# Kernel optimization log

Hardware: AMD Instinct MI355X
Metric: run time of the kernel (lower is better)

The kernel has to match this reference:

```python
import jax, jax.numpy as jnp
import numpy as np


def setup_inputs() -> dict:
    key = jax.random.key(0)
    k1, k2 = jax.random.split(key)
    from_points = jax.random.normal(k1, (16384, 64), dtype=jnp.float32)
    to_points = jax.random.normal(k2, (16384, 64), dtype=jnp.float32)
    return {"from_points": from_points, "to_points": to_points}


def reference(from_points, to_points):
    # Squared L2 distance matrix [N, M] via ||a||^2 + ||b||^2 - 2 a.b,
    # avoiding the O(N*M*D) broadcasted intermediate of the original.
    a_sq = jnp.sum(from_points * from_points, axis=-1)          # [N]
    b_sq = jnp.sum(to_points * to_points, axis=-1)              # [M]
    cross = jnp.einsum('nd,md->nm', from_points, to_points)     # [N, M]
    dist_mat = a_sq[:, None] + b_sq[None, :] - 2.0 * cross      # [N, M]
    # Row-wise min (nearest neighbor squared distance), then sum.
    return jnp.sum(jnp.min(dist_mat, axis=1))
```

## Files before the change

### kernel.cpp

```cpp
#include <hip/hip_runtime.h>
#include <stdint.h>

#define N_PTS 16384
#define TSPLITS 32
#define NBLOCKS (256 * TSPLITS / 4)
#define TO_TILES 16

typedef __attribute__((ext_vector_type(8)))  short bf16x8;
typedef __attribute__((ext_vector_type(16))) float f32x16;

__device__ __forceinline__ unsigned short f2bf(float f) {
    unsigned u = __float_as_uint(f);
    u += 0x7FFFu + ((u >> 16) & 1u);
    return (unsigned short)(u >> 16);
}
__device__ __forceinline__ float tree16(f32x16 a) {
    float m0 = fminf(fminf(a[0],  a[1]),  a[2]);
    float m1 = fminf(fminf(a[3],  a[4]),  a[5]);
    float m2 = fminf(fminf(a[6],  a[7]),  a[8]);
    float m3 = fminf(fminf(a[9],  a[10]), a[11]);
    float m4 = fminf(fminf(a[12], a[13]), a[14]);
    float m5 = fminf(fminf(a[15], m0), m1);
    return fminf(fminf(fminf(m2, m3), m4), m5);
}

__global__ __launch_bounds__(256) void prep_kernel(
        const float* __restrict__ from_pts, const float* __restrict__ to_pts,
        float* __restrict__ a_sq, float* __restrict__ bsqp,
        unsigned short* __restrict__ BfF, unsigned short* __restrict__ AtoF,
        float* __restrict__ out) {
    int gid = blockIdx.x * 256 + threadIdx.x;
    int row = gid >> 3;
    int sub = gid & 7;
    bool isFrom = row < N_PTS;
    int r = row & (N_PTS - 1);
    const float* src = isFrom ? from_pts : to_pts;
    float4 v0 = ((const float4*)src)[r * 16 + sub * 2];
    float4 v1 = ((const float4*)src)[r * 16 + sub * 2 + 1];
    float s = v0.x*v0.x + v0.y*v0.y + v0.z*v0.z + v0.w*v0.w
            + v1.x*v1.x + v1.y*v1.y + v1.z*v1.z + v1.w*v1.w;
    s += __shfl_xor(s, 1); s += __shfl_xor(s, 2); s += __shfl_xor(s, 4);
    float sc = isFrom ? -2.0f : 1.0f;
    union { unsigned short u[8]; uint4 q; } w;
    w.u[0] = f2bf(v0.x * sc); w.u[1] = f2bf(v0.y * sc);
    w.u[2] = f2bf(v0.z * sc); w.u[3] = f2bf(v0.w * sc);
    w.u[4] = f2bf(v1.x * sc); w.u[5] = f2bf(v1.y * sc);
    w.u[6] = f2bf(v1.z * sc); w.u[7] = f2bf(v1.w * sc);
    int st = r >> 5;
    int m  = r & 31;
    int kb = sub >> 1, h = sub & 1;
    size_t fidx = (((size_t)st * 4 + kb) * 64 + h * 32 + m) * 8;
    if (isFrom) {
        *(uint4*)(BfF + fidx) = w.q;
        if (sub == 0) a_sq[r] = s;
    } else {
        *(uint4*)(AtoF + fidx) = w.q;
        if (sub == 0)
            bsqp[st * 32 + ((m >> 2) & 1) * 16 + (m & 3) + 4 * (m >> 3)] = s;
    }
    if (gid == 0) out[0] = 0.0f;
}

__global__ __launch_bounds__(256, 4) void main_kernel(
        const unsigned short* __restrict__ BfF,
        const unsigned short* __restrict__ AtoF,
        const float* __restrict__ bsqp, float* __restrict__ pmin) {
    __shared__ __align__(16) unsigned short abuf[2][2048];
    __shared__ __align__(16) float bsq_s[512];

    const int tid = threadIdx.x;
    const int lane = tid & 63;
    const int l31 = lane & 31;
    const int h   = lane >> 5;
    const int wv  = tid >> 6;
    const int wid = (blockIdx.x << 2) + wv;
    const int fg  = wid & 255;
    const int ts  = wid >> 8;

    const bf16x8* Bv = (const bf16x8*)BfF;

    bsq_s[tid]       = bsqp[ts * 512 + tid];
    bsq_s[tid + 256] = bsqp[ts * 512 + 256 + tid];

    bf16x8 Bf0[4], Bf1[4];
    #pragma unroll
    for (int kb = 0; kb < 4; kb++) {
        Bf0[kb] = Bv[((size_t)(2 * fg)     * 4 + kb) * 64 + lane];
        Bf1[kb] = Bv[((size_t)(2 * fg + 1) * 4 + kb) * 64 + lane];
    }

    const int gtb = ts * TO_TILES;
    auto stage = [&](int gt, int buf) {
        const unsigned short* g = AtoF + (((size_t)gt * 4 + wv) * 64 + lane) * 8;
        unsigned short* l = &abuf[buf][wv * 512];
        __builtin_amdgcn_global_load_lds(
            (const __attribute__((address_space(1))) unsigned int*)g,
            (__attribute__((address_space(3))) unsigned int*)l, 16, 0, 0);
    };

    float rmin0 = 3.0e38f, rmin1 = 3.0e38f;
    auto compute = [&](int tl, int cb) {
        bf16x8 A[4];
        #pragma unroll
        for (int kb = 0; kb < 4; kb++)
            A[kb] = *(const bf16x8*)&abuf[cb][kb * 512 + lane * 8];
        union { float4 f[4]; f32x16 v; } cu;
        const float4* cp = (const float4*)&bsq_s[tl * 32 + h * 16];
        cu.f[0] = cp[0]; cu.f[1] = cp[1]; cu.f[2] = cp[2]; cu.f[3] = cp[3];
        f32x16 acc0 = __builtin_amdgcn_mfma_f32_32x32x16_bf16(A[0], Bf0[0], cu.v, 0, 0, 0);
        acc0 = __builtin_amdgcn_mfma_f32_32x32x16_bf16(A[1], Bf0[1], acc0, 0, 0, 0);
        acc0 = __builtin_amdgcn_mfma_f32_32x32x16_bf16(A[2], Bf0[2], acc0, 0, 0, 0);
        acc0 = __builtin_amdgcn_mfma_f32_32x32x16_bf16(A[3], Bf0[3], acc0, 0, 0, 0);
        rmin0 = fminf(rmin0, tree16(acc0));
        f32x16 acc1 = __builtin_amdgcn_mfma_f32_32x32x16_bf16(A[0], Bf1[0], cu.v, 0, 0, 0);
        acc1 = __builtin_amdgcn_mfma_f32_32x32x16_bf16(A[1], Bf1[1], acc1, 0, 0, 0);
        acc1 = __builtin_amdgcn_mfma_f32_32x32x16_bf16(A[2], Bf1[2], acc1, 0, 0, 0);
        acc1 = __builtin_amdgcn_mfma_f32_32x32x16_bf16(A[3], Bf1[3], acc1, 0, 0, 0);
        rmin1 = fminf(rmin1, tree16(acc1));
    };

    stage(gtb, 0);
    __syncthreads();
    #pragma unroll 1
    for (int t = 0; t < TO_TILES - 1; t++) {
        stage(gtb + t + 1, (t + 1) & 1);
        compute(t, t & 1);
        __syncthreads();
    }
    compute(TO_TILES - 1, (TO_TILES - 1) & 1);

    rmin0 = fminf(rmin0, __shfl_xor(rmin0, 32));
    rmin1 = fminf(rmin1, __shfl_xor(rmin1, 32));
    if (lane < 32) {
        pmin[(size_t)ts * N_PTS + fg * 64 + l31]      = rmin0;
        pmin[(size_t)ts * N_PTS + fg * 64 + 32 + l31] = rmin1;
    }
}

__global__ __launch_bounds__(256) void finish_kernel(
        const float* __restrict__ a_sq, const float* __restrict__ pmin,
        float* __restrict__ out) {
    int r = blockIdx.x * 256 + threadIdx.x;
    float m = pmin[r];
    #pragma unroll
    for (int s = 1; s < TSPLITS; s++)
        m = fminf(m, pmin[(size_t)s * N_PTS + r]);
    float v = a_sq[r] + m;
    #pragma unroll
    for (int k = 1; k < 64; k <<= 1) v += __shfl_xor(v, k);
    __shared__ float red[4];
    if ((threadIdx.x & 63) == 0) red[threadIdx.x >> 6] = v;
    __syncthreads();
    if (threadIdx.x == 0)
        atomicAdd(out, red[0] + red[1] + red[2] + red[3]);
}

extern "C" void kernel_launch(void* const* d_in, const int* in_sizes, int n_in,
                              void* d_out, int out_size, void* d_ws, size_t ws_size,
                              hipStream_t stream) {
    const float* from_pts = (const float*)d_in[0];
    const float* to_pts   = (const float*)d_in[1];
    char* ws = (char*)d_ws;
    float*          a_sq = (float*)ws;
    float*          bsqp = (float*)(ws + (64 << 10));
    float*          pmin = (float*)(ws + (128 << 10));
    unsigned short* BfF  = (unsigned short*)(ws + (128 << 10) + (2 << 20));
    unsigned short* AtoF = (unsigned short*)(ws + (128 << 10) + (2 << 20) + (2 << 20));

    prep_kernel<<<(2 * N_PTS * 8) / 256, 256, 0, stream>>>(
        from_pts, to_pts, a_sq, bsqp, BfF, AtoF, (float*)d_out);
    main_kernel<<<NBLOCKS, 256, 0, stream>>>(BfF, AtoF, bsqp, pmin);
    finish_kernel<<<N_PTS / 256, 256, 0, stream>>>(a_sq, pmin, (float*)d_out);
}
```

Measured before the change: 92.60 us.

## Stage whole to-point slice in LDS once and reuse across more from-groups

Each block now has 512 threads and loads its entire 512-point to-slice (64 KB of bf16) into LDS once, with a single barrier, replacing the per-tile double-buffered staging. Each wave processes two from-groups sequentially against that resident slice, so the LDS data is reused by 16 from-groups per block instead of 4, and the per-tile __syncthreads is removed. The bsq bias is read directly from global memory instead of shared. In exchange, the 64 KB LDS footprint limits how many blocks fit per CU, and the initial load is exposed with no overlap.

After: 94.87 us. 2.5% more time.

```diff
diff --git a/kernel.cpp b/kernel.cpp
--- a/kernel.cpp
+++ b/kernel.cpp
@@ -3,8 +3,9 @@
 
 #define N_PTS 16384
 #define TSPLITS 32
-#define NBLOCKS (256 * TSPLITS / 4)
 #define TO_TILES 16
+#define FGPB 16
+#define NBLOCKS (TSPLITS * (256 / FGPB))
 
 typedef __attribute__((ext_vector_type(8)))  short bf16x8;
 typedef __attribute__((ext_vector_type(16))) float f32x16;
@@ -61,79 +62,74 @@
     if (gid == 0) out[0] = 0.0f;
 }
 
-__global__ __launch_bounds__(256, 4) void main_kernel(
+__global__ __launch_bounds__(512, 4) void main_kernel(
         const unsigned short* __restrict__ BfF,
         const unsigned short* __restrict__ AtoF,
         const float* __restrict__ bsqp, float* __restrict__ pmin) {
-    __shared__ __align__(16) unsigned short abuf[2][2048];
-    __shared__ __align__(16) float bsq_s[512];
+    __shared__ __align__(16) unsigned short abuf[32768];
 
     const int tid = threadIdx.x;
     const int lane = tid & 63;
     const int l31 = lane & 31;
     const int h   = lane >> 5;
     const int wv  = tid >> 6;
-    const int wid = (blockIdx.x << 2) + wv;
-    const int fg  = wid & 255;
-    const int ts  = wid >> 8;
+    const int ts  = blockIdx.x >> 4;
+    const int bg  = blockIdx.x & 15;
+    const int gtb = ts * TO_TILES;
+
+    #pragma unroll
+    for (int j2 = 0; j2 < 8; j2++) {
+        int j  = wv * 8 + j2;
+        const unsigned short* g =
+            AtoF + (((size_t)(gtb + (j >> 2)) * 4 + (j & 3)) * 64 + lane) * 8;
+        unsigned short* l = &abuf[j * 512];
+        __builtin_amdgcn_global_load_lds(
+            (const __attribute__((address_space(1))) unsigned int*)g,
+            (__attribute__((address_space(3))) unsigned int*)l, 16, 0, 0);
+    }
+    __syncthreads();
 
     const bf16x8* Bv = (const bf16x8*)BfF;
 
-    bsq_s[tid]       = bsqp[ts * 512 + tid];
-    bsq_s[tid + 256] = bsqp[ts * 512 + 256 + tid];
+    #pragma unroll 1
+    for (int f2 = 0; f2 < 2; f2++) {
+        const int fg = bg * FGPB + f2 * 8 + wv;
+        bf16x8 Bf0[4], Bf1[4];
+        #pragma unroll
+        for (int kb = 0; kb < 4; kb++) {
+            Bf0[kb] = Bv[((size_t)(2 * fg)     * 4 + kb) * 64 + lane];
+            Bf1[kb] = Bv[((size_t)(2 * fg + 1) * 4 + kb) * 64 + lane];
+        }
+        float rmin0 = 3.0e38f, rmin1 = 3.0e38f;
 
-    bf16x8 Bf0[4], Bf1[4];
-    #pragma unroll
-    for (int kb = 0; kb < 4; kb++) {
-        Bf0[kb] = Bv[((size_t)(2 * fg)     * 4 + kb) * 64 + lane];
-        Bf1[kb] = Bv[((size_t)(2 * fg + 1) * 4 + kb) * 64 + lane];
-    }
+        #pragma unroll 1
+        for (int t = 0; t < TO_TILES; t++) {
+            bf16x8 A[4];
+            #pragma unroll
+            for (int kb = 0; kb < 4; kb++)
+                A[kb] = *(const bf16x8*)&abuf[(t * 4 + kb) * 512 + lane * 8];
+            union { float4 f[4]; f32x16 v; } cu;
+            const float4* cp = (const float4*)(bsqp + (gtb + t) * 32 + h * 16);
+            cu.f[0] = cp[0]; cu.f[1] = cp[1]; cu.f[2] = cp[2]; cu.f[3] = cp[3];
 
-    const int gtb = ts * TO_TILES;
-    auto stage = [&](int gt, int buf) {
-        const unsigned short* g = AtoF + (((size_t)gt * 4 + wv) * 64 + lane) * 8;
-        unsigned short* l = &abuf[buf][wv * 512];
-        __builtin_amdgcn_global_load_lds(
-            (const __attribute__((address_space(1))) unsigned int*)g,
-            (__attribute__((address_space(3))) unsigned int*)l, 16, 0, 0);
-    };
+            f32x16 acc0 = __builtin_amdgcn_mfma_f32_32x32x16_bf16(A[0], Bf0[0], cu.v, 0, 0, 0);
+            acc0 = __builtin_amdgcn_mfma_f32_32x32x16_bf16(A[1], Bf0[1], acc0, 0, 0, 0);
+            acc0 = __builtin_amdgcn_mfma_f32_32x32x16_bf16(A[2], Bf0[2], acc0, 0, 0, 0);
+            acc0 = __builtin_amdgcn_mfma_f32_32x32x16_bf16(A[3], Bf0[3], acc0, 0, 0, 0);
+            rmin0 = fminf(rmin0, tree16(acc0));
+            f32x16 acc1 = __builtin_amdgcn_mfma_f32_32x32x16_bf16(A[0], Bf1[0], cu.v, 0, 0, 0);
+            acc1 = __builtin_amdgcn_mfma_f32_32x32x16_bf16(A[1], Bf1[1], acc1, 0, 0, 0);
+            acc1 = __builtin_amdgcn_mfma_f32_32x32x16_bf16(A[2], Bf1[2], acc1, 0, 0, 0);
+            acc1 = __builtin_amdgcn_mfma_f32_32x32x16_bf16(A[3], Bf1[3], acc1, 0, 0, 0);
+            rmin1 = fminf(rmin1, tree16(acc1));
+        }
 
-    float rmin0 = 3.0e38f, rmin1 = 3.0e38f;
-    auto compute = [&](int tl, int cb) {
-        bf16x8 A[4];
-        #pragma unroll
-        for (int kb = 0; kb < 4; kb++)
-            A[kb] = *(const bf16x8*)&abuf[cb][kb * 512 + lane * 8];
-        union { float4 f[4]; f32x16 v; } cu;
-        const float4* cp = (const float4*)&bsq_s[tl * 32 + h * 16];
-        cu.f[0] = cp[0]; cu.f[1] = cp[1]; cu.f[2] = cp[2]; cu.f[3] = cp[3];
-        f32x16 acc0 = __builtin_amdgcn_mfma_f32_32x32x16_bf16(A[0], Bf0[0], cu.v, 0, 0, 0);
-        acc0 = __builtin_amdgcn_mfma_f32_32x32x16_bf16(A[1], Bf0[1], acc0, 0, 0, 0);
-        acc0 = __builtin_amdgcn_mfma_f32_32x32x16_bf16(A[2], Bf0[2], acc0, 0, 0, 0);
-        acc0 = __builtin_amdgcn_mfma_f32_32x32x16_bf16(A[3], Bf0[3], acc0, 0, 0, 0);
-        rmin0 = fminf(rmin0, tree16(acc0));
-        f32x16 acc1 = __builtin_amdgcn_mfma_f32_32x32x16_bf16(A[0], Bf1[0], cu.v, 0, 0, 0);
-        acc1 = __builtin_amdgcn_mfma_f32_32x32x16_bf16(A[1], Bf1[1], acc1, 0, 0, 0);
-        acc1 = __builtin_amdgcn_mfma_f32_32x32x16_bf16(A[2], Bf1[2], acc1, 0, 0, 0);
-        acc1 = __builtin_amdgcn_mfma_f32_32x32x16_bf16(A[3], Bf1[3], acc1, 0, 0, 0);
-        rmin1 = fminf(rmin1, tree16(acc1));
-    };
-
-    stage(gtb, 0);
-    __syncthreads();
-    #pragma unroll 1
-    for (int t = 0; t < TO_TILES - 1; t++) {
-        stage(gtb + t + 1, (t + 1) & 1);
-        compute(t, t & 1);
-        __syncthreads();
-    }
-    compute(TO_TILES - 1, (TO_TILES - 1) & 1);
-
-    rmin0 = fminf(rmin0, __shfl_xor(rmin0, 32));
-    rmin1 = fminf(rmin1, __shfl_xor(rmin1, 32));
-    if (lane < 32) {
-        pmin[(size_t)ts * N_PTS + fg * 64 + l31]      = rmin0;
-        pmin[(size_t)ts * N_PTS + fg * 64 + 32 + l31] = rmin1;
+        rmin0 = fminf(rmin0, __shfl_xor(rmin0, 32));
+        rmin1 = fminf(rmin1, __shfl_xor(rmin1, 32));
+        if (lane < 32) {
+            pmin[(size_t)ts * N_PTS + fg * 64 + l31]      = rmin0;
+            pmin[(size_t)ts * N_PTS + fg * 64 + 32 + l31] = rmin1;
+        }
     }
 }
 
@@ -169,6 +165,6 @@
 
     prep_kernel<<<(2 * N_PTS * 8) / 256, 256, 0, stream>>>(
         from_pts, to_pts, a_sq, bsqp, BfF, AtoF, (float*)d_out);
-    main_kernel<<<NBLOCKS, 256, 0, stream>>>(BfF, AtoF, bsqp, pmin);
+    main_kernel<<<NBLOCKS, 512, 0, stream>>>(BfF, AtoF, bsqp, pmin);
     finish_kernel<<<N_PTS / 256, 256, 0, stream>>>(a_sq, pmin, (float*)d_out);
 }
```
